# Performance work log

Hardware: AMD Instinct MI355X
Metric: run time of the kernel (lower is better)

Reference implementation:

```python
import jax, jax.numpy as jnp
import numpy as np

B, N0, D0 = 256, 64, 128
N1, D1 = 64, 128


def setup_inputs() -> dict:
    key = jax.random.key(0)
    k1, k2 = jax.random.split(key)
    x = jax.random.normal(k1, (B, N0, D0), dtype=jnp.float32)
    # kaiming_normal_ (fan_in mode): fan_in = N0 * D0 * D1 for a [N1,N0,D0,D1] tensor
    std = np.sqrt(2.0 / (N0 * D0 * D1)).astype(np.float32)
    W = jax.random.normal(k2, (N1, N0, D0, D1), dtype=jnp.float32) * std
    b = jnp.zeros((N1, N0, 1), dtype=jnp.float32)
    return {"x": x, "W": W, "b": b}


def reference(x, W, b):
    u = jnp.einsum('bji,kjiz->bkjz', x, W)  # [B, N1, N0, D1]
    # c[b, n1, i] = sum_{k,j} u[b,n1,i,j] * u[b,n1,k,j] = u[b,n1,i,:] . sum_k u[b,n1,k,:]
    s = jnp.sum(u, axis=-2)                      # [B, N1, D1]
    c = jnp.einsum('bkjz,bkz->bkj', u, s)        # [B, N1, N0]
    c = c[..., None] / jnp.sqrt(jnp.asarray(u.shape[-1], dtype=u.dtype))
    c = jax.nn.softmax(c, axis=1)                # softmax over N1 (absolute axis 1)
    c = c + b
    return jnp.sum(u * c, axis=-2)               # [B, N1, D1]
```

## Files before the change

### kernel.cpp

```cpp
#include <hip/hip_runtime.h>
#include <hip/hip_bf16.h>
#include <cstdint>


#define BB 256
#define NN0 64
#define DD0 128
#define NN1 64
#define DD1 128

typedef __attribute__((ext_vector_type(8))) short bf16x8;
typedef __attribute__((ext_vector_type(4))) float f32x4;

__device__ __forceinline__ ushort f2bf(float f) {
  uint32_t b = __float_as_uint(f);
  b += 0x7FFFu + ((b >> 16) & 1u);
  return (ushort)(b >> 16);
}
__device__ __forceinline__ float bf2f(ushort h) {
  return __uint_as_float(((uint32_t)h) << 16);
}

__device__ __forceinline__ void gld_lds16(const void* g, void* l) {
  __builtin_amdgcn_global_load_lds(
      (const __attribute__((address_space(1))) void*)g,
      (__attribute__((address_space(3))) void*)l, 16, 0, 0);
}

__device__ __forceinline__ void bar_lgkm() {
  asm volatile("s_waitcnt lgkmcnt(0)" ::: "memory");
  __builtin_amdgcn_s_barrier();
  __builtin_amdgcn_sched_barrier(0);
}

__global__ __launch_bounds__(512) void px_cvt(
    const float* __restrict__ x, ushort* __restrict__ xbf)
{
  int i = blockIdx.x * 512 + threadIdx.x;
  const f32x4* src = reinterpret_cast<const f32x4*>(x) + i;
  f32x4 v = __builtin_nontemporal_load(src);
  ushort4 h;
  h.x = f2bf(v.x); h.y = f2bf(v.y); h.z = f2bf(v.z); h.w = f2bf(v.w);
  *reinterpret_cast<ushort4*>(xbf + (size_t)i * 4) = h;
}

__global__ __launch_bounds__(512, 4) void k1_gemm(
    const ushort* __restrict__ xbf, const float* __restrict__ W,
    ushort* __restrict__ u)
{
  __shared__ __align__(16) char lds[81920];
  char* Alds = lds;
  char* Bl[2] = { lds + 65536, lds + 73728 };

  const int q = blockIdx.x;
  const int local = q >> 3;
  const int n0 = (q & 7) * 8 + (local >> 6);
  const int n1 = local & 63;
  const int t = threadIdx.x;
  const int lane = t & 63, wave = t >> 6;
  const int wm = wave >> 1, wn = wave & 1;

  const ushort* xb = xbf + n0 * DD0;
  const float* Wb = W + ((size_t)n1 * NN0 + n0) * (DD0 * DD1);
  ushort* ub = u + ((size_t)n1 * 8192 + (size_t)n0 * 128);

  f32x4 acc[4][4];
#pragma unroll
  for (int a = 0; a < 4; ++a)
#pragma unroll
    for (int b = 0; b < 4; ++b) acc[a][b] = {0.f, 0.f, 0.f, 0.f};

  const int gd1 = t & 127, gkc = t >> 7;
  const int bbyte = (gd1 * 64 + gkc * 16) ^ ((gd1 & 3) << 4) ^ (((gd1 >> 2) & 1) << 6);
  float w0[8], w1[8];

#define LOADW(hh, ks)                                                         \
  {                                                                           \
    _Pragma("unroll")                                                         \
    for (int j = 0; j < 8; ++j)                                               \
      hh[j] = __builtin_nontemporal_load(                                     \
          Wb + (size_t)((ks) * 32 + gkc * 8 + j) * 128 + gd1);                \
  }
#define PACKB(bi, hh)                                                         \
  {                                                                           \
    uint32_t p0 = (uint32_t)f2bf(hh[0]) | ((uint32_t)f2bf(hh[1]) << 16);      \
    uint32_t p1 = (uint32_t)f2bf(hh[2]) | ((uint32_t)f2bf(hh[3]) << 16);      \
    uint32_t p2 = (uint32_t)f2bf(hh[4]) | ((uint32_t)f2bf(hh[5]) << 16);      \
    uint32_t p3 = (uint32_t)f2bf(hh[6]) | ((uint32_t)f2bf(hh[7]) << 16);      \
    *reinterpret_cast<uint4*>(Bl[bi] + bbyte) = make_uint4(p0, p1, p2, p3);   \
  }
#define MFMA_STEP(ks, bi)                                                     \
  {                                                                           \
    const int kb16 = (lane >> 4);                                             \
    const int ka = (ks) * 32 + kb16 * 8;                                      \
    bf16x8 af[4], bfr[4];                                                     \
    _Pragma("unroll")                                                         \
    for (int mf = 0; mf < 4; ++mf) {                                          \
      int row = wm * 64 + mf * 16 + (lane & 15);                              \
      int byte = (row * 256 + ka * 2) ^ ((row & 7) << 4);                     \
      af[mf] = *reinterpret_cast<const bf16x8*>(Alds + byte);                 \
    }                                                                         \
    _Pragma("unroll")                                                         \
    for (int nf = 0; nf < 4; ++nf) {                                          \
      int n = wn * 64 + nf * 16 + (lane & 15);                                \
      int byte = (n * 64 + kb16 * 16) ^ ((n & 3) << 4) ^ (((n >> 2) & 1) << 6); \
      bfr[nf] = *reinterpret_cast<const bf16x8*>(Bl[bi] + byte);              \
    }                                                                         \
    _Pragma("unroll")                                                         \
    for (int mf = 0; mf < 4; ++mf)                                            \
      _Pragma("unroll")                                                       \
      for (int nf = 0; nf < 4; ++nf)                                          \
        acc[mf][nf] = __builtin_amdgcn_mfma_f32_16x16x32_bf16(af[mf], bfr[nf], acc[mf][nf], 0, 0, 0); \
  }

#pragma unroll
  for (int s = 0; s < 8; ++s) {
    int seg = wave * 8 + s;
    int row = seg * 4 + (lane >> 4);
    int srcc = (lane & 15) ^ (row & 7);
    gld_lds16(xb + (size_t)row * 8192 + srcc * 8, Alds + seg * 1024);
  }
  __builtin_amdgcn_sched_barrier(0);
  LOADW(w0, 0);
  __builtin_amdgcn_sched_barrier(0);
  LOADW(w1, 1);
  __builtin_amdgcn_sched_barrier(0);
  PACKB(0, w0);
  LOADW(w0, 2);
  __builtin_amdgcn_sched_barrier(0);
  bar_lgkm();

  PACKB(1, w1);
  LOADW(w1, 3);
  __builtin_amdgcn_sched_barrier(0);
  MFMA_STEP(0, 0);
  bar_lgkm();

  PACKB(0, w0);
  __builtin_amdgcn_sched_barrier(0);
  MFMA_STEP(1, 1);
  bar_lgkm();

  PACKB(1, w1);
  __builtin_amdgcn_sched_barrier(0);
  MFMA_STEP(2, 0);
  bar_lgkm();

  MFMA_STEP(3, 1);

  bar_lgkm();
#pragma unroll
  for (int mf = 0; mf < 4; ++mf) {
#pragma unroll
    for (int nf = 0; nf < 4; ++nf) {
      int col = wn * 64 + nf * 16 + (lane & 15);
#pragma unroll
      for (int j = 0; j < 4; ++j) {
        int rr = wm * 64 + mf * 16 + (lane >> 4) * 4 + j;
        int byte = (rr * 256 + col * 2) ^ ((rr & 7) << 4);
        *reinterpret_cast<ushort*>(Alds + byte) = f2bf(acc[mf][nf][j]);
      }
    }
  }
  bar_lgkm();
#pragma unroll
  for (int ci = 0; ci < 8; ++ci) {
    int c = t + ci * 512;
    int rowl = c >> 4;
    int cb = (c & 15) * 16;
    int sbyte = (rowl * 256 + cb) ^ ((rowl & 7) << 4);
    uint4 v = *reinterpret_cast<uint4*>(Alds + sbyte);
    *reinterpret_cast<uint4*>(ub + (size_t)rowl * 524288 + cb / 2) = v;
  }
#undef LOADW
#undef PACKB
#undef MFMA_STEP
}

__global__ __launch_bounds__(512, 1) void k234_fused(
    const ushort* __restrict__ u, const float* __restrict__ bias,
    float* __restrict__ out)
{
  const int b = blockIdx.x;
  const ushort* ub = u + (size_t)b * 524288;
  const int t = threadIdx.x;
  const int lane = t & 63, w = t >> 6;

  __shared__ float cL[64][65];
  __shared__ float red[2][8][64];

#pragma unroll 1
  for (int i = 0; i < 8; ++i) {
    const int n1 = w * 8 + i;
    const ushort* row = ub + n1 * 8192 + lane * 2;
    float s0 = 0.f, s1 = 0.f;
#pragma unroll
    for (int n0 = 0; n0 < 64; ++n0) {
      uint32_t v = *reinterpret_cast<const uint32_t*>(row + n0 * 128);
      s0 += bf2f((ushort)(v & 0xffff));
      s1 += bf2f((ushort)(v >> 16));
    }
    float p[64];
#pragma unroll
    for (int n0 = 0; n0 < 64; ++n0) {
      uint32_t v = *reinterpret_cast<const uint32_t*>(row + n0 * 128);
      p[n0] = bf2f((ushort)(v & 0xffff)) * s0 + bf2f((ushort)(v >> 16)) * s1;
    }
#pragma unroll
    for (int s2 = 0; s2 < 6; ++s2) {
      const int kb = (lane >> s2) & 1;
#pragma unroll
      for (int j = 0; j < (64 >> (s2 + 1)); ++j) {
        float a = p[2 * j], b2 = p[2 * j + 1];
        float mine = kb ? b2 : a;
        float send = kb ? a : b2;
        p[j] = mine + __shfl_xor(send, 1 << s2, 64);
      }
    }
    cL[n1][lane] = p[0] * 0.08838834764831845f;
  }
  __syncthreads();

  {
    const int g = t >> 6, n0 = t & 63;
    float pm = -1e30f;
#pragma unroll
    for (int j = 0; j < 8; ++j) pm = fmaxf(pm, cL[g * 8 + j][n0]);
    red[0][g][n0] = pm;
    __syncthreads();
    if (g == 0) {
      float m = red[0][0][n0];
#pragma unroll
      for (int j = 1; j < 8; ++j) m = fmaxf(m, red[0][j][n0]);
      red[0][0][n0] = m;
    }
    __syncthreads();
    const float m = red[0][0][n0];
    float ps = 0.f;
#pragma unroll
    for (int j = 0; j < 8; ++j) {
      float e = __expf(cL[g * 8 + j][n0] - m);
      cL[g * 8 + j][n0] = e;
      ps += e;
    }
    red[1][g][n0] = ps;
    __syncthreads();
    if (g == 0) {
      float sm = 0.f;
#pragma unroll
      for (int j = 0; j < 8; ++j) sm += red[1][j][n0];
      red[1][0][n0] = 1.0f / sm;
    }
    __syncthreads();
    const float inv = red[1][0][n0];
#pragma unroll
    for (int j = 0; j < 8; ++j) {
      int n1 = g * 8 + j;
      cL[n1][n0] = cL[n1][n0] * inv + bias[n1 * 64 + n0];
    }
  }
  __syncthreads();

#pragma unroll 1
  for (int i = 0; i < 8; ++i) {
    const int n1 = w * 8 + i;
    const ushort* row = ub + n1 * 8192 + lane * 2;
    float o0 = 0.f, o1 = 0.f;
#pragma unroll
    for (int n0 = 0; n0 < 64; ++n0) {
      uint32_t v = *reinterpret_cast<const uint32_t*>(row + n0 * 128);
      float c = cL[n1][n0];
      o0 += bf2f((ushort)(v & 0xffff)) * c;
      o1 += bf2f((ushort)(v >> 16)) * c;
    }
    float2 o = make_float2(o0, o1);
    *reinterpret_cast<float2*>(out + (size_t)b * 8192 + n1 * 128 + lane * 2) = o;
  }
}

extern "C" void kernel_launch(void* const* d_in, const int* in_sizes, int n_in,
                              void* d_out, int out_size, void* d_ws, size_t ws_size,
                              hipStream_t stream) {
  const float* x = (const float*)d_in[0];
  const float* W = (const float*)d_in[1];
  const float* bias = (const float*)d_in[2];
  float* out = (float*)d_out;

  ushort* u = (ushort*)d_ws;
  ushort* xbf = (ushort*)((char*)d_ws + 268435456u);

  hipLaunchKernelGGL(px_cvt,     dim3(1024), dim3(512), 0, stream, x, xbf);
  hipLaunchKernelGGL(k1_gemm,    dim3(4096), dim3(512), 0, stream, xbf, W, u);
  hipLaunchKernelGGL(k234_fused, dim3(BB),   dim3(512), 0, stream, u, bias, out);
}
```

Baseline: 183.1 us.

## Vectorize fused softmax-reduction kernel with 16-byte loads and register-resident rows

Rewrites the per-row work in the fused k234 kernel so each lane loads 16-byte bf16x8 vectors. A wavefront covers 4 n0 rows per step, holding all 16 loaded vectors in registers so u is read once for both the column sum and the dot product, not twice. The cross-lane reductions are restructured to match, and the output is written with 128-bit stores. Launch bounds are raised to allow two blocks per CU. The cost is higher register pressure from the 16 held vectors, which may conflict with the occupancy target and cause spills.

```diff
diff --git a/kernel.cpp b/kernel.cpp
--- a/kernel.cpp
+++ b/kernel.cpp
@@ -177,7 +177,7 @@
 #undef MFMA_STEP
 }
 
-__global__ __launch_bounds__(512, 1) void k234_fused(
+__global__ __launch_bounds__(512, 2) void k234_fused(
     const ushort* __restrict__ u, const float* __restrict__ bias,
     float* __restrict__ out)
 {
@@ -185,6 +185,7 @@
   const ushort* ub = u + (size_t)b * 524288;
   const int t = threadIdx.x;
   const int lane = t & 63, w = t >> 6;
+  const int g = lane >> 4, c = lane & 15;
 
   __shared__ float cL[64][65];
   __shared__ float red[2][8][64];
@@ -192,43 +193,55 @@
 #pragma unroll 1
   for (int i = 0; i < 8; ++i) {
     const int n1 = w * 8 + i;
-    const ushort* row = ub + n1 * 8192 + lane * 2;
-    float s0 = 0.f, s1 = 0.f;
-#pragma unroll
-    for (int n0 = 0; n0 < 64; ++n0) {
-      uint32_t v = *reinterpret_cast<const uint32_t*>(row + n0 * 128);
-      s0 += bf2f((ushort)(v & 0xffff));
-      s1 += bf2f((ushort)(v >> 16));
-    }
-    float p[64];
-#pragma unroll
-    for (int n0 = 0; n0 < 64; ++n0) {
-      uint32_t v = *reinterpret_cast<const uint32_t*>(row + n0 * 128);
-      p[n0] = bf2f((ushort)(v & 0xffff)) * s0 + bf2f((ushort)(v >> 16)) * s1;
-    }
-#pragma unroll
-    for (int s2 = 0; s2 < 6; ++s2) {
-      const int kb = (lane >> s2) & 1;
-#pragma unroll
-      for (int j = 0; j < (64 >> (s2 + 1)); ++j) {
+    const ushort* base = ub + n1 * 8192 + g * 128 + c * 8;
+    bf16x8 rows[16];
+#pragma unroll
+    for (int q = 0; q < 16; ++q)
+      rows[q] = *reinterpret_cast<const bf16x8*>(base + q * 512);
+
+    float s8[8];
+#pragma unroll
+    for (int j = 0; j < 8; ++j) s8[j] = 0.f;
+#pragma unroll
+    for (int q = 0; q < 16; ++q)
+#pragma unroll
+      for (int j = 0; j < 8; ++j) s8[j] += bf2f((ushort)rows[q][j]);
+#pragma unroll
+    for (int j = 0; j < 8; ++j) {
+      s8[j] += __shfl_xor(s8[j], 16, 64);
+      s8[j] += __shfl_xor(s8[j], 32, 64);
+    }
+    float p[16];
+#pragma unroll
+    for (int q = 0; q < 16; ++q) {
+      float a = 0.f;
+#pragma unroll
+      for (int j = 0; j < 8; ++j) a += bf2f((ushort)rows[q][j]) * s8[j];
+      p[q] = a;
+    }
+#pragma unroll
+    for (int s2 = 0; s2 < 4; ++s2) {
+      const int kb = (c >> s2) & 1;
+#pragma unroll
+      for (int j = 0; j < (16 >> (s2 + 1)); ++j) {
         float a = p[2 * j], b2 = p[2 * j + 1];
         float mine = kb ? b2 : a;
         float send = kb ? a : b2;
         p[j] = mine + __shfl_xor(send, 1 << s2, 64);
       }
     }
-    cL[n1][lane] = p[0] * 0.08838834764831845f;
+    cL[n1][c * 4 + g] = p[0] * 0.08838834764831845f;
   }
   __syncthreads();
 
   {
-    const int g = t >> 6, n0 = t & 63;
+    const int gg = t >> 6, n0 = t & 63;
     float pm = -1e30f;
 #pragma unroll
-    for (int j = 0; j < 8; ++j) pm = fmaxf(pm, cL[g * 8 + j][n0]);
-    red[0][g][n0] = pm;
+    for (int j = 0; j < 8; ++j) pm = fmaxf(pm, cL[gg * 8 + j][n0]);
+    red[0][gg][n0] = pm;
     __syncthreads();
-    if (g == 0) {
+    if (gg == 0) {
       float m = red[0][0][n0];
 #pragma unroll
       for (int j = 1; j < 8; ++j) m = fmaxf(m, red[0][j][n0]);
@@ -239,13 +252,13 @@
     float ps = 0.f;
 #pragma unroll
     for (int j = 0; j < 8; ++j) {
-      float e = __expf(cL[g * 8 + j][n0] - m);
-      cL[g * 8 + j][n0] = e;
+      float e = __expf(cL[gg * 8 + j][n0] - m);
+      cL[gg * 8 + j][n0] = e;
       ps += e;
     }
-    red[1][g][n0] = ps;
+    red[1][gg][n0] = ps;
     __syncthreads();
-    if (g == 0) {
+    if (gg == 0) {
       float sm = 0.f;
 #pragma unroll
       for (int j = 0; j < 8; ++j) sm += red[1][j][n0];
@@ -255,7 +268,7 @@
     const float inv = red[1][0][n0];
 #pragma unroll
     for (int j = 0; j < 8; ++j) {
-      int n1 = g * 8 + j;
+      int n1 = gg * 8 + j;
       cL[n1][n0] = cL[n1][n0] * inv + bias[n1 * 64 + n0];
     }
   }
@@ -264,17 +277,29 @@
 #pragma unroll 1
   for (int i = 0; i < 8; ++i) {
     const int n1 = w * 8 + i;
-    const ushort* row = ub + n1 * 8192 + lane * 2;
-    float o0 = 0.f, o1 = 0.f;
-#pragma unroll
-    for (int n0 = 0; n0 < 64; ++n0) {
-      uint32_t v = *reinterpret_cast<const uint32_t*>(row + n0 * 128);
-      float c = cL[n1][n0];
-      o0 += bf2f((ushort)(v & 0xffff)) * c;
-      o1 += bf2f((ushort)(v >> 16)) * c;
-    }
-    float2 o = make_float2(o0, o1);
-    *reinterpret_cast<float2*>(out + (size_t)b * 8192 + n1 * 128 + lane * 2) = o;
+    const ushort* base = ub + n1 * 8192 + g * 128 + c * 8;
+    float o8[8];
+#pragma unroll
+    for (int j = 0; j < 8; ++j) o8[j] = 0.f;
+#pragma unroll
+    for (int q = 0; q < 16; ++q) {
+      bf16x8 v = *reinterpret_cast<const bf16x8*>(base + q * 512);
+      float cc = cL[n1][q * 4 + g];
+#pragma unroll
+      for (int j = 0; j < 8; ++j) o8[j] += bf2f((ushort)v[j]) * cc;
+    }
+#pragma unroll
+    for (int j = 0; j < 8; ++j) {
+      o8[j] += __shfl_xor(o8[j], 16, 64);
+      o8[j] += __shfl_xor(o8[j], 32, 64);
+    }
+    if (g == 0) {
+      float* op = out + (size_t)b * 8192 + n1 * 128 + c * 8;
+      f32x4 v0 = {o8[0], o8[1], o8[2], o8[3]};
+      f32x4 v1 = {o8[4], o8[5], o8[6], o8[7]};
+      *reinterpret_cast<f32x4*>(op) = v0;
+      *reinterpret_cast<f32x4*>(op + 4) = v1;
+    }
   }
 }
 
```

New measurement: 180.9 us. No clear change (-1.2%).
